# Kernel tuning notes

Measured on AMD Instinct MI355X. Metric: run time of the kernel, lower is better.

## Reference

```python
import jax, jax.numpy as jnp
import numpy as np
import math

B, S, E = 4, 2048, 1024


def setup_inputs() -> dict:
    key = jax.random.key(0)
    ks = jax.random.split(key, 9)
    x = jax.random.normal(ks[0], (B, S, E), dtype=jnp.float32)
    # causal boolean mask, broadcast over batch: True = keep
    mask = jnp.broadcast_to(jnp.tril(jnp.ones((S, S), dtype=bool)), (B, S, S))
    sc = 1.0 / math.sqrt(E)
    Wq = jax.random.normal(ks[1], (E, E), dtype=jnp.float32) * sc
    bq = jnp.zeros((E,), dtype=jnp.float32)
    Wk = jax.random.normal(ks[2], (E, E), dtype=jnp.float32) * sc
    bk = jnp.zeros((E,), dtype=jnp.float32)
    Wv = jax.random.normal(ks[3], (E, E), dtype=jnp.float32) * sc
    bv = jnp.zeros((E,), dtype=jnp.float32)
    gamma = jnp.ones((E,), dtype=jnp.float32)
    beta = jnp.zeros((E,), dtype=jnp.float32)
    return {"x": x, "mask": mask, "Wq": Wq, "bq": bq, "Wk": Wk, "bk": bk,
            "Wv": Wv, "bv": bv, "gamma": gamma, "beta": beta}


def reference(x, mask, Wq, bq, Wk, bk, Wv, bv, gamma, beta):
    E_ = x.shape[-1]
    q = jnp.einsum('bse,fe->bsf', x, Wq) + bq
    k = jnp.einsum('bse,fe->bsf', x, Wk) + bk
    v = jnp.einsum('bse,fe->bsf', x, Wv) + bv
    scores = jnp.einsum('bqe,bke->bqk', q, k) / jnp.sqrt(jnp.float32(E_))
    scores = jnp.where(mask, scores, -jnp.inf)
    probs = jax.nn.softmax(scores, axis=-1)
    attn = jnp.einsum('bqk,bke->bqe', probs, v)
    y = attn + x
    # LayerNorm over last dim, eps matches torch default 1e-5
    mu = jnp.mean(y, axis=-1, keepdims=True)
    var = jnp.mean(jnp.square(y - mu), axis=-1, keepdims=True)
    return (y - mu) / jnp.sqrt(var + 1e-5) * gamma + beta
```

## Files before the change

kernel.cpp:

```cpp
#include <hip/hip_runtime.h>
#include <hip/hip_bf16.h>
#include <stdint.h>

#define B_ 4
#define S_ 2048
#define E_ 1024
#define BS_ (B_*S_)

using bf16x8 = __attribute__((ext_vector_type(8))) __bf16;
using f32x4  = __attribute__((ext_vector_type(4))) float;

__constant__ int pv_mt[24] = {7,8,9,10,11,12,13,14,15,15,14,6,13,5,12,4,11,3,10,2,9,1,8,0};
__constant__ int pv_ck[24] = {0,0,0,0,0,0,0,0,0, 1, 1,0, 1,0, 1,0, 1,0, 1,0, 1,0, 1,0};

__device__ __forceinline__ unsigned short f2bf(float f) {
  unsigned int u = __float_as_uint(f);
  u += 0x7fffu + ((u >> 16) & 1u);
  return (unsigned short)(u >> 16);
}
__device__ __forceinline__ float bf2f(unsigned short h) {
  return __uint_as_float(((unsigned int)h) << 16);
}

__device__ __forceinline__ void gld16(const unsigned short* g, unsigned short* l) {
  __builtin_amdgcn_global_load_lds((__attribute__((address_space(1))) void*)(void*)g,
                                   (__attribute__((address_space(3))) void*)l, 16, 0, 0);
}

__global__ __launch_bounds__(256) void prep_all(
    const float* __restrict__ x,
    const float* __restrict__ Wq, const float* __restrict__ Wk, const float* __restrict__ Wv,
    const float* __restrict__ bq, const float* __restrict__ bk, const float* __restrict__ bv,
    unsigned short* __restrict__ xb, unsigned short* __restrict__ Wb, float* __restrict__ bb) {
  const int i = blockIdx.x * 256 + threadIdx.x;
  const int nx4 = BS_ * E_ / 4, nw4 = E_ * E_ / 4;
  if (i < nx4) {
    const float4 v = ((const float4*)x)[i];
    ushort4 o;
    o.x = f2bf(v.x); o.y = f2bf(v.y); o.z = f2bf(v.z); o.w = f2bf(v.w);
    ((ushort4*)xb)[i] = o;
  } else if (i < nx4 + 3 * nw4) {
    const int j = i - nx4;
    const int m = j / nw4, jj = j - m * nw4;
    const float* src = (m == 0) ? Wq : (m == 1) ? Wk : Wv;
    const float4 v = ((const float4*)src)[jj];
    ushort4 o;
    o.x = f2bf(v.x); o.y = f2bf(v.y); o.z = f2bf(v.z); o.w = f2bf(v.w);
    ((ushort4*)Wb)[j] = o;
  } else {
    const int j = i - nx4 - 3 * nw4;
    if (j < 3 * E_) bb[j] = (j < E_) ? bq[j] : (j < 2 * E_) ? bk[j - E_] : bv[j - 2 * E_];
  }
}

template<int EPI>
__global__ __launch_bounds__(256, 3) void gemm_bt(
    const unsigned short* __restrict__ A, const unsigned short* __restrict__ Bm,
    float* __restrict__ Cf, float* __restrict__ Cf2,
    unsigned short* __restrict__ Cb, unsigned short* __restrict__ VtOut,
    const float* __restrict__ bias,
    int K, int lda, int ldb, int ldc,
    long sA, long sB, long sC, float scale)
{
  constexpr int BM = 128, BN = 128, BK = 64;
  __shared__ __align__(16) unsigned short As[BM * BK];
  __shared__ __align__(16) unsigned short Bs[BN * BK];
  const int bz = blockIdx.z;
  A  += sA * bz;
  Bm += sB * bz;

  int mt, nt, ck = 0;
  if (EPI == 1) {
    const int id = blockIdx.x;
    mt = (int)((sqrtf(8.f * id + 1.f) - 1.f) * 0.5f);
    while ((mt * (mt + 1)) / 2 > id) --mt;
    while (((mt + 1) * (mt + 2)) / 2 <= id) ++mt;
    nt = id - (mt * (mt + 1)) / 2;
  } else if (EPI == 2) {
    mt = pv_mt[blockIdx.y]; ck = pv_ck[blockIdx.y]; nt = blockIdx.x;
  } else {
    mt = blockIdx.y; nt = blockIdx.x;
  }
  const int m0 = mt * BM, n0 = nt * BN;
  const int k0s  = (EPI == 2 && ck) ? 1024 : 0;
  const int kend = (EPI == 2) ? (ck ? m0 + BM : min(1024, m0 + BM)) : K;

  const int t = threadIdx.x;
  const int lane = t & 63, wave = t >> 6;
  const int wr = wave >> 1, wc = wave & 1;
  const int q = lane >> 4, r = lane & 15;

  const int srow   = lane >> 3;
  const int schunk = (lane & 7) ^ srow;
  const long ga0 = (long)(m0 + wave * 32 + srow) * lda + schunk * 8;
  const long gb0 = (long)(n0 + wave * 32 + srow) * ldb + schunk * 8;

  f32x4 acc[4][4] = {};

  for (int k0 = k0s; k0 < kend; k0 += BK) {
#pragma unroll
    for (int s = 0; s < 4; ++s) {
      gld16(A  + ga0 + (long)s * 8 * lda + k0, &As[(wave * 32 + s * 8) * 64]);
      gld16(Bm + gb0 + (long)s * 8 * ldb + k0, &Bs[(wave * 32 + s * 8) * 64]);
    }
    __syncthreads();
#pragma unroll
    for (int kk = 0; kk < BK; kk += 32) {
      bf16x8 af[4], bfr[4];
      const int cq = (kk >> 3) + q;
#pragma unroll
      for (int i = 0; i < 4; ++i) {
        const int row = wr * 64 + i * 16 + r;
        af[i] = *(const bf16x8*)&As[(row * 8 + (cq ^ (r & 7))) * 8];
      }
#pragma unroll
      for (int j = 0; j < 4; ++j) {
        const int row = wc * 64 + j * 16 + r;
        bfr[j] = *(const bf16x8*)&Bs[(row * 8 + (cq ^ (r & 7))) * 8];
      }
#pragma unroll
      for (int i = 0; i < 4; ++i)
#pragma unroll
        for (int j = 0; j < 4; ++j)
          acc[i][j] = __builtin_amdgcn_mfma_f32_16x16x32_bf16(af[i], bfr[j], acc[i][j], 0, 0, 0);
    }
    __syncthreads();
  }

  if (EPI == 0) {
    if (n0 < 2 * E_) {
#pragma unroll
      for (int i = 0; i < 4; ++i)
#pragma unroll
        for (int j = 0; j < 4; ++j) {
          const int col = n0 + wc * 64 + j * 16 + r;
          const float bia = bias[col];
#pragma unroll
          for (int e = 0; e < 4; ++e) {
            const int rowg = m0 + wr * 64 + i * 16 + q * 4 + e;
            Cb[(long)rowg * ldc + col] = f2bf(acc[i][j][e] + bia);
          }
        }
    } else {
#pragma unroll
      for (int i = 0; i < 4; ++i) {
        const int base = m0 + wr * 64 + i * 16 + q * 4;
        const int b = base >> 11, s0 = base & (S_ - 1);
#pragma unroll
        for (int j = 0; j < 4; ++j) {
          const int col = n0 + wc * 64 + j * 16 + r;
          const int e_ = col - 2 * E_;
          const float bia = bias[col];
          ushort4 o;
          o.x = f2bf(acc[i][j][0] + bia);
          o.y = f2bf(acc[i][j][1] + bia);
          o.z = f2bf(acc[i][j][2] + bia);
          o.w = f2bf(acc[i][j][3] + bia);
          *(ushort4*)&VtOut[((long)b * E_ + e_) * S_ + s0] = o;
        }
      }
    }
  } else if (EPI == 1) {
    Cb += sC * bz;
#pragma unroll
    for (int i = 0; i < 4; ++i)
#pragma unroll
      for (int j = 0; j < 4; ++j) {
        const int col = n0 + wc * 64 + j * 16 + r;
#pragma unroll
        for (int e = 0; e < 4; ++e) {
          const int rowg = m0 + wr * 64 + i * 16 + q * 4 + e;
          Cb[(long)rowg * ldc + col] = f2bf(acc[i][j][e] * scale);
        }
      }
  } else {
    float* dst = (ck ? Cf2 : Cf) + sC * bz;
#pragma unroll
    for (int i = 0; i < 4; ++i)
#pragma unroll
      for (int j = 0; j < 4; ++j) {
        const int col = n0 + wc * 64 + j * 16 + r;
#pragma unroll
        for (int e = 0; e < 4; ++e) {
          const int rowg = m0 + wr * 64 + i * 16 + q * 4 + e;
          dst[(long)rowg * ldc + col] = acc[i][j][e];
        }
      }
  }
}

__global__ __launch_bounds__(256) void softmax_causal(unsigned short* __restrict__ Sc) {
  const int row = blockIdx.x * 4 + (threadIdx.x >> 6);
  const int lane = threadIdx.x & 63;
  const int b = row >> 11, ii = row & (S_ - 1);
  unsigned short* prow = Sc + (long)b * S_ * S_ + (long)ii * S_;
  const int len = ii + 1;
  const int wend = ((ii >> 7) + 1) << 7;
  float v[32];
#pragma unroll
  for (int c = 0; c < 4; ++c) {
    const int base = (c * 64 + lane) * 8;
    if (base < len) {
      const uint4 u = *(const uint4*)&prow[base];
      const unsigned int w[4] = {u.x, u.y, u.z, u.w};
#pragma unroll
      for (int e = 0; e < 8; ++e) {
        const unsigned short h = (unsigned short)(w[e >> 1] >> ((e & 1) * 16));
        v[c * 8 + e] = (base + e < len) ? bf2f(h) : -3.0e38f;
      }
    } else {
#pragma unroll
      for (int e = 0; e < 8; ++e) v[c * 8 + e] = -3.0e38f;
    }
  }
  float mx = -3.0e38f;
#pragma unroll
  for (int i = 0; i < 32; ++i) mx = fmaxf(mx, v[i]);
#pragma unroll
  for (int o = 32; o; o >>= 1) mx = fmaxf(mx, __shfl_xor(mx, o));
  float sum = 0.f;
#pragma unroll
  for (int i = 0; i < 32; ++i) { v[i] = __expf(v[i] - mx); sum += v[i]; }
#pragma unroll
  for (int o = 32; o; o >>= 1) sum += __shfl_xor(sum, o);
  const float inv = 1.0f / sum;
#pragma unroll
  for (int c = 0; c < 4; ++c) {
    const int base = (c * 64 + lane) * 8;
    if (base >= wend) continue;
    uint4 u;
    unsigned int w[4];
#pragma unroll
    for (int p = 0; p < 4; ++p) {
      const unsigned short lo = f2bf(v[c * 8 + p * 2] * inv);
      const unsigned short hi = f2bf(v[c * 8 + p * 2 + 1] * inv);
      w[p] = (unsigned int)lo | ((unsigned int)hi << 16);
    }
    u.x = w[0]; u.y = w[1]; u.z = w[2]; u.w = w[3];
    *(uint4*)&prow[base] = u;
  }
}

__global__ __launch_bounds__(256) void residual_ln(
    const float* __restrict__ attn, const float* __restrict__ attn2,
    const float* __restrict__ x,
    const float* __restrict__ gamma, const float* __restrict__ beta,
    float* __restrict__ out) {
  __shared__ float rs[4], rs2[4];
  const long row = blockIdx.x;
  const int t = threadIdx.x;
  const int lane = t & 63, wave = t >> 6;
  const float4 a  = ((const float4*)(attn + row * E_))[t];
  const float4 xv = ((const float4*)(x + row * E_))[t];
  float4 a2 = make_float4(0.f, 0.f, 0.f, 0.f);
  if ((row & (S_ - 1)) >= 1024) a2 = ((const float4*)(attn2 + row * E_))[t];
  const float y0 = a.x + a2.x + xv.x, y1 = a.y + a2.y + xv.y;
  const float y2 = a.z + a2.z + xv.z, y3 = a.w + a2.w + xv.w;
  float s  = y0 + y1 + y2 + y3;
  float s2 = y0 * y0 + y1 * y1 + y2 * y2 + y3 * y3;
#pragma unroll
  for (int o = 32; o; o >>= 1) { s += __shfl_xor(s, o); s2 += __shfl_xor(s2, o); }
  if (lane == 0) { rs[wave] = s; rs2[wave] = s2; }
  __syncthreads();
  s  = rs[0] + rs[1] + rs[2] + rs[3];
  s2 = rs2[0] + rs2[1] + rs2[2] + rs2[3];
  const float mu  = s * (1.0f / E_);
  const float var = s2 * (1.0f / E_) - mu * mu;
  const float inv = rsqrtf(var + 1e-5f);
  const float4 g  = ((const float4*)gamma)[t];
  const float4 be = ((const float4*)beta)[t];
  float4 o;
  o.x = (y0 - mu) * inv * g.x + be.x;
  o.y = (y1 - mu) * inv * g.y + be.y;
  o.z = (y2 - mu) * inv * g.z + be.z;
  o.w = (y3 - mu) * inv * g.w + be.w;
  ((float4*)(out + row * E_))[t] = o;
}

extern "C" void kernel_launch(void* const* d_in, const int* in_sizes, int n_in,
                              void* d_out, int out_size, void* d_ws, size_t ws_size,
                              hipStream_t stream) {
  const float* x  = (const float*)d_in[0];
  const float* Wq = (const float*)d_in[2];
  const float* bq = (const float*)d_in[3];
  const float* Wk = (const float*)d_in[4];
  const float* bk = (const float*)d_in[5];
  const float* Wv = (const float*)d_in[6];
  const float* bv = (const float*)d_in[7];
  const float* gamma = (const float*)d_in[8];
  const float* beta  = (const float*)d_in[9];
  float* out = (float*)d_out;

  char* ws = (char*)d_ws;
  size_t off = 0;
  auto alloc = [&](size_t bytes) { char* p = ws + off; off += (bytes + 255) & ~(size_t)255; return p; };
  unsigned short* xb    = (unsigned short*)alloc((size_t)BS_ * E_ * 2);
  unsigned short* Wqkvb = (unsigned short*)alloc((size_t)3 * E_ * E_ * 2);
  float*          bqkv  = (float*)alloc((size_t)3 * E_ * 4);
  unsigned short* Cqkv  = (unsigned short*)alloc((size_t)BS_ * 2 * E_ * 2);
  unsigned short* Vt    = (unsigned short*)alloc((size_t)BS_ * E_ * 2);
  unsigned short* Sc    = (unsigned short*)alloc((size_t)B_ * S_ * S_ * 2);
  float*          attn2 = (float*)alloc((size_t)BS_ * E_ * 4);
  float* attn = (float*)Cqkv;

  const int nprep = BS_ * E_ / 4 + 3 * E_ * E_ / 4 + 3 * E_;
  prep_all<<<dim3((nprep + 255) / 256), 256, 0, stream>>>(x, Wq, Wk, Wv, bq, bk, bv, xb, Wqkvb, bqkv);

  dim3 g1(3 * E_ / 128, BS_ / 128, 1);
  gemm_bt<0><<<g1, 256, 0, stream>>>(xb, Wqkvb, nullptr, nullptr, Cqkv, Vt, bqkv,
                                     E_, E_, E_, 2 * E_, 0, 0, 0, 1.f);

  dim3 g2(136, 1, B_);
  gemm_bt<1><<<g2, 256, 0, stream>>>(Cqkv, Cqkv + E_, nullptr, nullptr, Sc, nullptr, nullptr,
                                     E_, 2 * E_, 2 * E_, S_,
                                     (long)S_ * 2 * E_, (long)S_ * 2 * E_, (long)S_ * S_, 0.03125f);

  softmax_causal<<<dim3(BS_ / 4), 256, 0, stream>>>(Sc);

  dim3 g3(E_ / 128, 24, B_);
  gemm_bt<2><<<g3, 256, 0, stream>>>(Sc, Vt, attn, attn2, nullptr, nullptr, nullptr,
                                     S_, S_, S_, E_,
                                     (long)S_ * S_, (long)S_ * E_, (long)S_ * E_, 1.f);

  residual_ln<<<dim3(BS_), 256, 0, stream>>>(attn, attn2, x, gamma, beta, out);
}
```

Measured before the change: 296.0 us.

## Swizzle QK^T block order into 4x4 supertiles and stage V-transpose stores via LDS

The causal QK^T GEMM now runs as a flat 544-block grid. Blocks are remapped so that consecutive blocks, spread across XCDs by the x&7 interleave, cover 4x4 groups of tiles within each batch, with the triangular diagonal groups handled separately. The aim is better L2 reuse of Q and K tiles. In the QKV projection epilogue, V-transposed output is first written into a swizzled LDS scratch region and then stored as 16-byte contiguous rows of Vt, replacing scattered 8-byte stores. This reuses the As buffer after the main loop, which relies on the final sync, and adds some index arithmetic.

New measurement: 277.1 us. 6.4% less time.

```diff
diff --git a/kernel.cpp b/kernel.cpp
--- a/kernel.cpp
+++ b/kernel.cpp
@@ -65,22 +65,31 @@
   constexpr int BM = 128, BN = 128, BK = 64;
   __shared__ __align__(16) unsigned short As[BM * BK];
   __shared__ __align__(16) unsigned short Bs[BN * BK];
-  const int bz = blockIdx.z;
+
+  int mt, nt, ck = 0, bz;
+  if (EPI == 1) {
+    const int sig = (blockIdx.x & 7) * 68 + (blockIdx.x >> 3);
+    bz = sig / 136;
+    const int rem = sig - bz * 136;
+    const int M = (rem >= 78) ? 3 : (rem >= 36) ? 2 : (rem >= 10) ? 1 : 0;
+    const int cumM = (M == 3) ? 78 : (M == 2) ? 36 : (M == 1) ? 10 : 0;
+    const int inner = rem - cumM;
+    if (inner < 16 * M) {
+      const int N = inner >> 4, t2 = inner & 15;
+      mt = 4 * M + (t2 >> 2); nt = 4 * N + (t2 & 3);
+    } else {
+      const int t2 = inner - 16 * M;
+      const int ml = (t2 >= 6) ? 3 : (t2 >= 3) ? 2 : (t2 >= 1) ? 1 : 0;
+      const int nl = t2 - (ml * (ml + 1)) / 2;
+      mt = 4 * M + ml; nt = 4 * M + nl;
+    }
+  } else if (EPI == 2) {
+    mt = pv_mt[blockIdx.y]; ck = pv_ck[blockIdx.y]; nt = blockIdx.x; bz = blockIdx.z;
+  } else {
+    mt = blockIdx.y; nt = blockIdx.x; bz = blockIdx.z;
+  }
   A  += sA * bz;
   Bm += sB * bz;
-
-  int mt, nt, ck = 0;
-  if (EPI == 1) {
-    const int id = blockIdx.x;
-    mt = (int)((sqrtf(8.f * id + 1.f) - 1.f) * 0.5f);
-    while ((mt * (mt + 1)) / 2 > id) --mt;
-    while (((mt + 1) * (mt + 2)) / 2 <= id) ++mt;
-    nt = id - (mt * (mt + 1)) / 2;
-  } else if (EPI == 2) {
-    mt = pv_mt[blockIdx.y]; ck = pv_ck[blockIdx.y]; nt = blockIdx.x;
-  } else {
-    mt = blockIdx.y; nt = blockIdx.x;
-  }
   const int m0 = mt * BM, n0 = nt * BN;
   const int k0s  = (EPI == 2 && ck) ? 1024 : 0;
   const int kend = (EPI == 2) ? (ck ? m0 + BM : min(1024, m0 + BM)) : K;
@@ -142,21 +151,33 @@
           }
         }
     } else {
-#pragma unroll
-      for (int i = 0; i < 4; ++i) {
-        const int base = m0 + wr * 64 + i * 16 + q * 4;
-        const int b = base >> 11, s0 = base & (S_ - 1);
-#pragma unroll
-        for (int j = 0; j < 4; ++j) {
-          const int col = n0 + wc * 64 + j * 16 + r;
-          const int e_ = col - 2 * E_;
-          const float bia = bias[col];
+      unsigned short* scr = As + wave * 2048;
+      const int bb = m0 >> 11;
+      const int sbase = (m0 & (S_ - 1)) + wr * 64;
+      const float bia = bias[n0 + wc * 64 +  0 + r];
+      (void)bia;
+#pragma unroll
+      for (int j = 0; j < 4; ++j) {
+        const int e_base = n0 - 2 * E_ + wc * 64 + j * 16;
+        const float bj = bias[n0 + wc * 64 + j * 16 + r];
+#pragma unroll
+        for (int i = 0; i < 4; ++i) {
+          const int c = 2 * i + (q >> 1);
+          const int slot = c ^ (r & 7);
           ushort4 o;
-          o.x = f2bf(acc[i][j][0] + bia);
-          o.y = f2bf(acc[i][j][1] + bia);
-          o.z = f2bf(acc[i][j][2] + bia);
-          o.w = f2bf(acc[i][j][3] + bia);
-          *(ushort4*)&VtOut[((long)b * E_ + e_) * S_ + s0] = o;
+          o.x = f2bf(acc[i][j][0] + bj);
+          o.y = f2bf(acc[i][j][1] + bj);
+          o.z = f2bf(acc[i][j][2] + bj);
+          o.w = f2bf(acc[i][j][3] + bj);
+          *(ushort4*)&scr[r * 72 + slot * 8 + (q & 1) * 4] = o;
+        }
+#pragma unroll
+        for (int it = 0; it < 2; ++it) {
+          const int er = it * 8 + (lane >> 3);
+          const int w = lane & 7;
+          const bf16x8 vv = *(const bf16x8*)&scr[er * 72 + w * 8];
+          const int so = (w ^ (er & 7)) * 8;
+          *(bf16x8*)&VtOut[((long)bb * E_ + e_base + er) * S_ + sbase + so] = vv;
         }
       }
     }
@@ -310,10 +331,10 @@
   gemm_bt<0><<<g1, 256, 0, stream>>>(xb, Wqkvb, nullptr, nullptr, Cqkv, Vt, bqkv,
                                      E_, E_, E_, 2 * E_, 0, 0, 0, 1.f);
 
-  dim3 g2(136, 1, B_);
-  gemm_bt<1><<<g2, 256, 0, stream>>>(Cqkv, Cqkv + E_, nullptr, nullptr, Sc, nullptr, nullptr,
-                                     E_, 2 * E_, 2 * E_, S_,
-                                     (long)S_ * 2 * E_, (long)S_ * 2 * E_, (long)S_ * S_, 0.03125f);
+  gemm_bt<1><<<dim3(544), 256, 0, stream>>>(Cqkv, Cqkv + E_, nullptr, nullptr, Sc, nullptr, nullptr,
+                                            E_, 2 * E_, 2 * E_, S_,
+                                            (long)S_ * 2 * E_, (long)S_ * 2 * E_, (long)S_ * S_,
+                                            0.03125f);
 
   softmax_causal<<<dim3(BS_ / 4), 256, 0, stream>>>(Sc);
 
```
